# Performance work log

Hardware: AMD Instinct MI355X
Metric: run time of the kernel (lower is better)

The kernel has to match this reference:

```python
import jax, jax.numpy as jnp
import numpy as np

B, T, S_ENC, D, H, E, K = 4, 1024, 64, 1024, 16, 8, 2
DK = D // H
HID = 4 * D
NEG = -65504.0
EPS = 1e-5


def rmsnorm(x, w):
    return w * (x * jax.lax.rsqrt(jnp.mean(x * x, axis=-1, keepdims=True) + EPS))


def mha(xq, xk, xv, mask, wq, wk, wv, wo):
    # linear (no bias): y = x @ W.T
    q = jnp.einsum('bsd,ed->bse', xq, wq).reshape(xq.shape[0], -1, H, DK).transpose(0, 2, 1, 3)
    k = jnp.einsum('bsd,ed->bse', xk, wk).reshape(xk.shape[0], -1, H, DK).transpose(0, 2, 1, 3)
    v = jnp.einsum('bsd,ed->bse', xv, wv).reshape(xv.shape[0], -1, H, DK).transpose(0, 2, 1, 3)
    scores = jnp.einsum('bhqd,bhkd->bhqk', q, k) / jnp.sqrt(jnp.float32(DK))
    scores = jnp.where(mask[:, None, :, :] == 0, NEG, scores)
    attn = jax.nn.softmax(scores, axis=-1)
    out = jnp.einsum('bhqk,bhkd->bhqd', attn, v)
    out = out.transpose(0, 2, 1, 3).reshape(xq.shape[0], -1, D)
    return jnp.einsum('bsd,ed->bse', out, wo)


def moe_ffn(x, gate_w, exp_w1, exp_w2, sh_w1, sh_w2):
    b, s, d = x.shape
    xf = x.reshape(-1, d)                                     # [N, D]
    # shared expert
    sh = jnp.einsum('nd,hd->nh', xf, sh_w1)
    sh = jax.nn.silu(sh)
    sh = jnp.einsum('nh,dh->nd', sh, sh_w2)
    # gating
    logits = jnp.einsum('nd,ed->ne', xf, gate_w)              # [N, E]
    topk_vals, topk_idx = jax.lax.top_k(logits, K)
    topk_gates = jax.nn.softmax(topk_vals, axis=-1)
    n = xf.shape[0]
    gates = jnp.zeros((n, E), dtype=xf.dtype).at[jnp.arange(n)[:, None], topk_idx].set(topk_gates)
    # all experts computed densely (as in the torch code), then gated
    h = jnp.einsum('nd,ehd->neh', xf, exp_w1)                 # [N, E, 4D]
    h = jax.nn.silu(h)
    eo = jnp.einsum('neh,edh->ned', h, exp_w2)                # [N, E, D]
    sel = jnp.einsum('ned,ne->nd', eo, gates)
    return (sh + sel).reshape(b, s, d)


def setup_inputs() -> dict:
    key = jax.random.key(0)
    ks = jax.random.split(key, 16)
    sd = 1.0 / np.sqrt(D)
    inp = {
        'x': jax.random.normal(ks[0], (B, T, D), jnp.float32),
        'encoder_output': jax.random.normal(ks[1], (B, S_ENC, D), jnp.float32),
        'tgt_mask': jnp.tril(jnp.ones((T, T), jnp.int32))[None].repeat(B, 0),
        'src_mask': jnp.ones((B, T, S_ENC), jnp.int32),
        'norm1_w': jnp.ones((D,), jnp.float32),
        'norm2_w': jnp.ones((D,), jnp.float32),
        'norm3_w': jnp.ones((D,), jnp.float32),
        'sa_wq': jax.random.normal(ks[2], (D, D), jnp.float32) * sd,
        'sa_wk': jax.random.normal(ks[3], (D, D), jnp.float32) * sd,
        'sa_wv': jax.random.normal(ks[4], (D, D), jnp.float32) * sd,
        'sa_wo': jax.random.normal(ks[5], (D, D), jnp.float32) * sd,
        'ca_wq': jax.random.normal(ks[6], (D, D), jnp.float32) * sd,
        'ca_wk': jax.random.normal(ks[7], (D, D), jnp.float32) * sd,
        'ca_wv': jax.random.normal(ks[8], (D, D), jnp.float32) * sd,
        'ca_wo': jax.random.normal(ks[9], (D, D), jnp.float32) * sd,
        'gate_w': jax.random.normal(ks[10], (E, D), jnp.float32) * 0.02,
        'exp_w1': jax.random.normal(ks[11], (E, HID, D), jnp.float32) * sd,
        'exp_w2': jax.random.normal(ks[12], (E, D, HID), jnp.float32) / np.sqrt(HID),
        'sh_w1': jax.random.normal(ks[13], (HID, D), jnp.float32) * sd,
        'sh_w2': jax.random.normal(ks[14], (D, HID), jnp.float32) / np.sqrt(HID),
    }
    return inp


def reference(x, encoder_output, tgt_mask, src_mask, norm1_w, norm2_w, norm3_w,
              sa_wq, sa_wk, sa_wv, sa_wo, ca_wq, ca_wk, ca_wv, ca_wo,
              gate_w, exp_w1, exp_w2, sh_w1, sh_w2):
    xn = rmsnorm(x, norm1_w)
    h = x + mha(xn, xn, xn, tgt_mask, sa_wq, sa_wk, sa_wv, sa_wo)
    hn = rmsnorm(h, norm2_w)
    h = h + mha(hn, encoder_output, encoder_output, src_mask, ca_wq, ca_wk, ca_wv, ca_wo)
    hn = rmsnorm(h, norm3_w)
    return h + moe_ffn(hn, gate_w, exp_w1, exp_w2, sh_w1, sh_w2)
```

## Files before the change

### kernel.cpp

```cpp
#include <hip/hip_runtime.h>
#include <hip/hip_bf16.h>
#include <cstdint>
#include <cstddef>
#include <math.h>

typedef __attribute__((ext_vector_type(8))) short bf16x8;
typedef __attribute__((ext_vector_type(4))) float f32x4;
typedef __attribute__((ext_vector_type(4))) short s16x4;

static __device__ __forceinline__ short f2bf(float f) {
  union { __hip_bfloat16 b; short s; } u;
  u.b = __float2bfloat16(f);
  return u.s;
}

static __device__ __forceinline__ float bf2f(short s) {
  union { unsigned u; float f; } v;
  v.u = ((unsigned)(unsigned short)s) << 16;
  return v.f;
}

static __device__ __forceinline__ void gload_lds16(const short* g, short* l) {
  __builtin_amdgcn_global_load_lds((const __attribute__((address_space(1))) void*)g,
                                   (__attribute__((address_space(3))) void*)l,
                                   16, 0, 0);
}

__global__ __launch_bounds__(256) void cvt_k(const float* __restrict__ src,
                                             short* __restrict__ dst, long n4) {
  long i = (long)blockIdx.x * blockDim.x + threadIdx.x;
  long stride = (long)gridDim.x * blockDim.x;
  for (; i < n4; i += stride) {
    float4 v = ((const float4*)src)[i];
    s16x4 o;
    o.x = f2bf(v.x); o.y = f2bf(v.y); o.z = f2bf(v.z); o.w = f2bf(v.w);
    ((s16x4*)dst)[i] = o;
  }
}

__global__ __launch_bounds__(256) void cvt2_k(const float* __restrict__ src,
                                              short* __restrict__ hi,
                                              short* __restrict__ lo, long n4) {
  long i = (long)blockIdx.x * blockDim.x + threadIdx.x;
  long stride = (long)gridDim.x * blockDim.x;
  for (; i < n4; i += stride) {
    float4 v = ((const float4*)src)[i];
    s16x4 h, l;
    h.x = f2bf(v.x); l.x = f2bf(v.x - bf2f(h.x));
    h.y = f2bf(v.y); l.y = f2bf(v.y - bf2f(h.y));
    h.z = f2bf(v.z); l.z = f2bf(v.z - bf2f(h.z));
    h.w = f2bf(v.w); l.w = f2bf(v.w - bf2f(h.w));
    ((s16x4*)hi)[i] = h;
    ((s16x4*)lo)[i] = l;
  }
}

__global__ __launch_bounds__(256) void rms2_k(const float* __restrict__ x,
                                              const float* __restrict__ w,
                                              short* __restrict__ hi,
                                              short* __restrict__ lo) {
  const int row = blockIdx.x, tid = threadIdx.x;
  const float* xr = x + (size_t)row * 1024;
  float4 v = *(const float4*)&xr[tid * 4];
  float ss = v.x * v.x + v.y * v.y + v.z * v.z + v.w * v.w;
#pragma unroll
  for (int off = 32; off; off >>= 1) ss += __shfl_down(ss, off);
  __shared__ float red[4];
  if ((tid & 63) == 0) red[tid >> 6] = ss;
  __syncthreads();
  float rs = rsqrtf((red[0] + red[1] + red[2] + red[3]) * (1.f / 1024.f) + 1e-5f);
  float4 wv = *(const float4*)&w[tid * 4];
  float o0 = v.x * rs * wv.x, o1 = v.y * rs * wv.y;
  float o2 = v.z * rs * wv.z, o3 = v.w * rs * wv.w;
  s16x4 h, l;
  h.x = f2bf(o0); l.x = f2bf(o0 - bf2f(h.x));
  h.y = f2bf(o1); l.y = f2bf(o1 - bf2f(h.y));
  h.z = f2bf(o2); l.z = f2bf(o2 - bf2f(h.z));
  h.w = f2bf(o3); l.w = f2bf(o3 - bf2f(h.w));
  const size_t ib = (size_t)row * 1024 + tid * 4;
  *(s16x4*)&hi[ib] = h;
  *(s16x4*)&lo[ib] = l;
}

__global__ __launch_bounds__(256) void rms_k(const float* __restrict__ x,
                                             const float* __restrict__ w,
                                             short* __restrict__ obf) {
  const int row = blockIdx.x, tid = threadIdx.x;
  const float* xr = x + (size_t)row * 1024;
  float4 v = *(const float4*)&xr[tid * 4];
  float ss = v.x * v.x + v.y * v.y + v.z * v.z + v.w * v.w;
#pragma unroll
  for (int off = 32; off; off >>= 1) ss += __shfl_down(ss, off);
  __shared__ float red[4];
  if ((tid & 63) == 0) red[tid >> 6] = ss;
  __syncthreads();
  float rs = rsqrtf((red[0] + red[1] + red[2] + red[3]) * (1.f / 1024.f) + 1e-5f);
  float4 wv = *(const float4*)&w[tid * 4];
  s16x4 ob;
  ob.x = f2bf(v.x * rs * wv.x); ob.y = f2bf(v.y * rs * wv.y);
  ob.z = f2bf(v.z * rs * wv.z); ob.w = f2bf(v.w * rs * wv.w);
  *(s16x4*)&obf[(size_t)row * 1024 + tid * 4] = ob;
}

template <int EPI>
__global__ __launch_bounds__(256)
void gemm3_k(const short* __restrict__ Ah, const short* __restrict__ Al,
             const short* __restrict__ Bh, const short* __restrict__ Bl,
             float* __restrict__ C, const float* __restrict__ resid,
             short* __restrict__ Ch, short* __restrict__ Cl,
             int M, int N, int K) {
  __shared__ short sAh[128 * 32];
  __shared__ short sAl[128 * 32];
  __shared__ short sBh[128 * 32];
  __shared__ short sBl[128 * 32];

  const int bn = blockIdx.x, bm = blockIdx.y;
  const int tid = threadIdx.x;
  const int lane = tid & 63, wv = tid >> 6;
  const int rch = lane >> 2, cch = (lane & 3) << 3;
  const int wr = wv >> 1, wc = wv & 1;
  const int lr = lane & 15, lg = lane >> 4;
  const int c0 = wv * 2, c1 = wv * 2 + 1;

  const int ra0 = bm * 128 + c0 * 16 + rch;
  const int ra1 = bm * 128 + c1 * 16 + rch;
  const int rb0 = bn * 128 + c0 * 16 + rch, rb1 = bn * 128 + c1 * 16 + rch;

  f32x4 acc[4][4];
#pragma unroll
  for (int m = 0; m < 4; m++)
#pragma unroll
    for (int n = 0; n < 4; n++) acc[m][n] = (f32x4){0.f, 0.f, 0.f, 0.f};

  const int nk = K >> 5;
  for (int kt = 0; kt < nk; ++kt) {
    __syncthreads();
    const int colk = (kt << 5) + cch;
    gload_lds16(Ah + (size_t)ra0 * K + colk, &sAh[c0 * 512]);
    gload_lds16(Ah + (size_t)ra1 * K + colk, &sAh[c1 * 512]);
    gload_lds16(Al + (size_t)ra0 * K + colk, &sAl[c0 * 512]);
    gload_lds16(Al + (size_t)ra1 * K + colk, &sAl[c1 * 512]);
    gload_lds16(Bh + (size_t)rb0 * K + colk, &sBh[c0 * 512]);
    gload_lds16(Bh + (size_t)rb1 * K + colk, &sBh[c1 * 512]);
    gload_lds16(Bl + (size_t)rb0 * K + colk, &sBl[c0 * 512]);
    gload_lds16(Bl + (size_t)rb1 * K + colk, &sBl[c1 * 512]);
    __syncthreads();
    bf16x8 ah[4], al[4], bh[4], bl[4];
#pragma unroll
    for (int m = 0; m < 4; m++) {
      const int o = (wr * 64 + m * 16 + lr) * 32 + lg * 8;
      ah[m] = *(const bf16x8*)&sAh[o];
      al[m] = *(const bf16x8*)&sAl[o];
    }
#pragma unroll
    for (int n = 0; n < 4; n++) {
      const int o = (wc * 64 + n * 16 + lr) * 32 + lg * 8;
      bh[n] = *(const bf16x8*)&sBh[o];
      bl[n] = *(const bf16x8*)&sBl[o];
    }
#pragma unroll
    for (int m = 0; m < 4; m++)
#pragma unroll
      for (int n = 0; n < 4; n++) {
        acc[m][n] = __builtin_amdgcn_mfma_f32_16x16x32_bf16(ah[m], bh[n], acc[m][n], 0, 0, 0);
        acc[m][n] = __builtin_amdgcn_mfma_f32_16x16x32_bf16(al[m], bh[n], acc[m][n], 0, 0, 0);
        acc[m][n] = __builtin_amdgcn_mfma_f32_16x16x32_bf16(ah[m], bl[n], acc[m][n], 0, 0, 0);
      }
  }

  const int cbase = bn * 128 + wc * 64;
#pragma unroll
  for (int m = 0; m < 4; m++) {
    const int rl = bm * 128 + wr * 64 + m * 16 + lg * 4;
#pragma unroll
    for (int n = 0; n < 4; n++) {
      f32x4 v = acc[m][n];
      const int col = cbase + n * 16 + lr;
#pragma unroll
      for (int j = 0; j < 4; j++) {
        const size_t idx = (size_t)(rl + j) * N + col;
        if (EPI == 0) {
          C[idx] = v[j];
        } else if (EPI == 2) {
          C[idx] = v[j] + resid[idx];
        } else {
          short hh = f2bf(v[j]);
          Ch[idx] = hh;
          Cl[idx] = f2bf(v[j] - bf2f(hh));
        }
      }
    }
  }
}

template <bool CAUSAL>
__global__ __launch_bounds__(256)
void attn3_k(const short* __restrict__ Qh, const short* __restrict__ Ql, int ldq,
             const short* __restrict__ Kh, const short* __restrict__ Kl, int ldk,
             const short* __restrict__ Vh, const short* __restrict__ Vl, int ldv,
             short* __restrict__ Oh, short* __restrict__ Ol, int ldo,
             int Tq, int Tkv, float scale) {
  __shared__ short sQh[64 * 64], sQl[64 * 64];
  __shared__ short sKh[64 * 64], sKl[64 * 64];
  __shared__ short sVh[64 * 72], sVl[64 * 72];
  __shared__ short sPh[4][16 * 72], sPl[4][16 * 72];

  const int idx = blockIdx.x;
  const int qb = 15 - (idx >> 6);
  const int h = (idx >> 2) & 15;
  const int b = idx & 3;
  const int tid = threadIdx.x, lane = tid & 63, wv = tid >> 6;
  const int hoff = h * 64;
  const int lr = lane & 15, lg = lane >> 4;
  const int qlo = wv * 16;

#pragma unroll
  for (int j = 0; j < 2; j++) {
    int c = j * 256 + tid;
    int row = c >> 3, col = (c & 7) << 3;
    size_t g = (size_t)(b * Tq + qb * 64 + row) * ldq + hoff + col;
    *(bf16x8*)&sQh[row * 64 + col] = *(const bf16x8*)&Qh[g];
    *(bf16x8*)&sQl[row * 64 + col] = *(const bf16x8*)&Ql[g];
  }

  float m_run = -1e30f, l_run = 0.f;
  f32x4 o[4];
#pragma unroll
  for (int n = 0; n < 4; n++) o[n] = (f32x4){0.f, 0.f, 0.f, 0.f};

  const int ntiles = CAUSAL ? (qb + 1) : (Tkv >> 6);
  for (int kt = 0; kt < ntiles; ++kt) {
    __syncthreads();
#pragma unroll
    for (int j = 0; j < 2; j++) {
      int c = j * 256 + tid;
      int row = c >> 3, col = (c & 7) << 3;
      size_t gk = (size_t)(b * Tkv + kt * 64 + row) * ldk + hoff + col;
      *(bf16x8*)&sKh[row * 64 + col] = *(const bf16x8*)&Kh[gk];
      *(bf16x8*)&sKl[row * 64 + col] = *(const bf16x8*)&Kl[gk];
      size_t gv = (size_t)(b * Tkv + kt * 64 + row) * ldv + hoff + col;
      bf16x8 vh = *(const bf16x8*)&Vh[gv];
      bf16x8 vl = *(const bf16x8*)&Vl[gv];
#pragma unroll
      for (int i = 0; i < 8; i++) {
        sVh[(col + i) * 72 + row] = vh[i];
        sVl[(col + i) * 72 + row] = vl[i];
      }
    }
    __syncthreads();

    f32x4 st[4];
#pragma unroll
    for (int jk = 0; jk < 4; jk++) st[jk] = (f32x4){0.f, 0.f, 0.f, 0.f};
#pragma unroll
    for (int ks = 0; ks < 2; ks++) {
      bf16x8 qh = *(const bf16x8*)&sQh[(qlo + lr) * 64 + ks * 32 + lg * 8];
      bf16x8 ql = *(const bf16x8*)&sQl[(qlo + lr) * 64 + ks * 32 + lg * 8];
#pragma unroll
      for (int jk = 0; jk < 4; jk++) {
        const int o2 = (jk * 16 + lr) * 64 + ks * 32 + lg * 8;
        bf16x8 kh = *(const bf16x8*)&sKh[o2];
        bf16x8 kl = *(const bf16x8*)&sKl[o2];
        st[jk] = __builtin_amdgcn_mfma_f32_16x16x32_bf16(kh, qh, st[jk], 0, 0, 0);
        st[jk] = __builtin_amdgcn_mfma_f32_16x16x32_bf16(kl, qh, st[jk], 0, 0, 0);
        st[jk] = __builtin_amdgcn_mfma_f32_16x16x32_bf16(kh, ql, st[jk], 0, 0, 0);
      }
    }

    const int qg = qb * 64 + qlo + lr;
    float s[16];
    float tmax = -1e30f;
#pragma unroll
    for (int jk = 0; jk < 4; jk++)
#pragma unroll
      for (int r2 = 0; r2 < 4; r2++) {
        float xv = st[jk][r2] * scale;
        if (CAUSAL && kt == qb) {
          int kvidx = kt * 64 + jk * 16 + lg * 4 + r2;
          if (kvidx > qg) xv = -1e30f;
        }
        s[jk * 4 + r2] = xv;
        tmax = fmaxf(tmax, xv);
      }
    tmax = fmaxf(tmax, __shfl_xor(tmax, 16));
    tmax = fmaxf(tmax, __shfl_xor(tmax, 32));
    float m_new = fmaxf(m_run, tmax);
    float alpha = __expf(m_run - m_new);
    float tsum = 0.f;
#pragma unroll
    for (int i = 0; i < 16; i++) {
      float ev = (s[i] <= -1e29f) ? 0.f : __expf(s[i] - m_new);
      s[i] = ev;
      tsum += ev;
    }
    tsum += __shfl_xor(tsum, 16);
    tsum += __shfl_xor(tsum, 32);
    l_run = l_run * alpha + tsum;
    m_run = m_new;

    short* pwh = &sPh[wv][0];
    short* pwl = &sPl[wv][0];
#pragma unroll
    for (int jk = 0; jk < 4; jk++) {
      s16x4 ph, pl;
      float e0 = s[jk * 4 + 0], e1 = s[jk * 4 + 1], e2 = s[jk * 4 + 2], e3 = s[jk * 4 + 3];
      ph.x = f2bf(e0); pl.x = f2bf(e0 - bf2f(ph.x));
      ph.y = f2bf(e1); pl.y = f2bf(e1 - bf2f(ph.y));
      ph.z = f2bf(e2); pl.z = f2bf(e2 - bf2f(ph.z));
      ph.w = f2bf(e3); pl.w = f2bf(e3 - bf2f(ph.w));
      *(s16x4*)&pwh[lr * 72 + jk * 16 + lg * 4] = ph;
      *(s16x4*)&pwl[lr * 72 + jk * 16 + lg * 4] = pl;
    }
#pragma unroll
    for (int r2 = 0; r2 < 4; r2++) {
      float al = __shfl(alpha, lg * 4 + r2);
#pragma unroll
      for (int db = 0; db < 4; db++) o[db][r2] *= al;
    }
    __syncthreads();

#pragma unroll
    for (int ks = 0; ks < 2; ks++) {
      bf16x8 pah = *(const bf16x8*)&pwh[lr * 72 + ks * 32 + lg * 8];
      bf16x8 pal = *(const bf16x8*)&pwl[lr * 72 + ks * 32 + lg * 8];
#pragma unroll
      for (int db = 0; db < 4; db++) {
        const int o2 = (db * 16 + lr) * 72 + ks * 32 + lg * 8;
        bf16x8 vfh = *(const bf16x8*)&sVh[o2];
        bf16x8 vfl = *(const bf16x8*)&sVl[o2];
        o[db] = __builtin_amdgcn_mfma_f32_16x16x32_bf16(pah, vfh, o[db], 0, 0, 0);
        o[db] = __builtin_amdgcn_mfma_f32_16x16x32_bf16(pal, vfh, o[db], 0, 0, 0);
        o[db] = __builtin_amdgcn_mfma_f32_16x16x32_bf16(pah, vfl, o[db], 0, 0, 0);
      }
    }
  }

  float rinv = 1.f / l_run;
#pragma unroll
  for (int r2 = 0; r2 < 4; r2++) {
    float inv = __shfl(rinv, lg * 4 + r2);
    int token = b * Tq + qb * 64 + qlo + lg * 4 + r2;
#pragma unroll
    for (int db = 0; db < 4; db++) {
      float vv = o[db][r2] * inv;
      short hh = f2bf(vv);
      const size_t ob = (size_t)token * ldo + hoff + db * 16 + lr;
      Oh[ob] = hh;
      Ol[ob] = f2bf(vv - bf2f(hh));
    }
  }
}

template <int EPI, int MODE>
__global__ __launch_bounds__(256)
void gemm_bt_k(const short* __restrict__ A, const short* __restrict__ B,
               void* C, int M, int N, int K,
               const int* __restrict__ row_map,
               const int* __restrict__ counts,
               const int* __restrict__ offs, int e0) {
  __shared__ short sA[128 * 32];
  __shared__ short sB[128 * 32];
  __shared__ int sRow[128];

  const int tid = threadIdx.x;
  const int bn = blockIdx.x, bm = blockIdx.y;
  const int e = e0 + blockIdx.z;
  const int cnt = counts[e];
  const int base = offs[e];
  if (bm * 128 >= cnt) return;
  const short* Bp = B + (size_t)e * N * K;

  const int lane = tid & 63, wv = tid >> 6;
  const int rch = lane >> 2, cch = (lane & 3) << 3;
  const int wr = wv >> 1, wc = wv & 1;
  const int lr = lane & 15, lg = lane >> 4;
  const int c0 = wv * 2, c1 = wv * 2 + 1;

  int ra0, ra1;
  if (MODE == 2) {
    int rl0 = bm * 128 + c0 * 16 + rch, rl1 = bm * 128 + c1 * 16 + rch;
    ra0 = base + ((rl0 < cnt) ? rl0 : 0);
    ra1 = base + ((rl1 < cnt) ? rl1 : 0);
  } else {
    if (tid < 128) {
      int r = bm * 128 + tid;
      sRow[tid] = (r < cnt) ? row_map[base + r] : row_map[base];
    }
    __syncthreads();
    ra0 = sRow[c0 * 16 + rch];
    ra1 = sRow[c1 * 16 + rch];
  }
  const int rb0 = bn * 128 + c0 * 16 + rch, rb1 = bn * 128 + c1 * 16 + rch;

  f32x4 acc[4][4];
#pragma unroll
  for (int m = 0; m < 4; m++)
#pragma unroll
    for (int n = 0; n < 4; n++) acc[m][n] = (f32x4){0.f, 0.f, 0.f, 0.f};

  const int nk = K >> 5;
  for (int kt = 0; kt < nk; ++kt) {
    __syncthreads();
    const int colk = (kt << 5) + cch;
    gload_lds16(A + (size_t)ra0 * K + colk, &sA[c0 * 512]);
    gload_lds16(A + (size_t)ra1 * K + colk, &sA[c1 * 512]);
    gload_lds16(Bp + (size_t)rb0 * K + colk, &sB[c0 * 512]);
    gload_lds16(Bp + (size_t)rb1 * K + colk, &sB[c1 * 512]);
    __syncthreads();
    bf16x8 a[4], b[4];
#pragma unroll
    for (int m = 0; m < 4; m++) a[m] = *(const bf16x8*)&sA[(wr * 64 + m * 16 + lr) * 32 + lg * 8];
#pragma unroll
    for (int n = 0; n < 4; n++) b[n] = *(const bf16x8*)&sB[(wc * 64 + n * 16 + lr) * 32 + lg * 8];
#pragma unroll
    for (int m = 0; m < 4; m++)
#pragma unroll
      for (int n = 0; n < 4; n++)
        acc[m][n] = __builtin_amdgcn_mfma_f32_16x16x32_bf16(a[m], b[n], acc[m][n], 0, 0, 0);
  }

  const int cbase = bn * 128 + wc * 64;
#pragma unroll
  for (int m = 0; m < 4; m++) {
    const int rl = wr * 64 + m * 16 + lg * 4;
#pragma unroll
    for (int n = 0; n < 4; n++) {
      f32x4 v = acc[m][n];
      const int col = cbase + n * 16 + lr;
#pragma unroll
      for (int j = 0; j < 4; j++) {
        const int rloc = bm * 128 + rl + j;
        if (rloc >= cnt) continue;
        const size_t idx = (size_t)(base + rloc) * N + col;
        float xv = v[j];
        if (EPI == 1) {
          float s = xv / (1.f + __expf(-xv));
          ((short*)C)[idx] = f2bf(s);
        } else {
          ((short*)C)[idx] = f2bf(xv);
        }
      }
    }
  }
}

__global__ __launch_bounds__(256) void gate_k(const float* __restrict__ H,
                                              const float* __restrict__ w3,
                                              const float* __restrict__ gw,
                                              int* counts, int* tok_e, int* tok_s,
                                              float* tok_g) {
  const int token = blockIdx.x * 4 + (threadIdx.x >> 6);
  const int lane = threadIdx.x & 63;
  const float* xr = H + (size_t)token * 1024;
  double a[8] = {0, 0, 0, 0, 0, 0, 0, 0};
  double ss = 0.0;
#pragma unroll
  for (int i = 0; i < 4; i++) {
    float4 xv = *(const float4*)&xr[i * 256 + lane * 4];
    float4 w3v = *(const float4*)&w3[i * 256 + lane * 4];
    ss += (double)xv.x * xv.x + (double)xv.y * xv.y + (double)xv.z * xv.z + (double)xv.w * xv.w;
    double xw0 = (double)xv.x * (double)w3v.x, xw1 = (double)xv.y * (double)w3v.y;
    double xw2 = (double)xv.z * (double)w3v.z, xw3 = (double)xv.w * (double)w3v.w;
#pragma unroll
    for (int e = 0; e < 8; e++) {
      float4 wv = *(const float4*)&gw[e * 1024 + i * 256 + lane * 4];
      a[e] += xw0 * wv.x + xw1 * wv.y + xw2 * wv.z + xw3 * wv.w;
    }
  }
#pragma unroll
  for (int off = 32; off; off >>= 1) {
    ss += __shfl_down(ss, off);
#pragma unroll
    for (int e = 0; e < 8; e++) a[e] += __shfl_down(a[e], off);
  }
  if (lane == 0) {
    double v0 = a[0]; int i0 = 0;
#pragma unroll
    for (int e = 1; e < 8; e++) if (a[e] > v0) { v0 = a[e]; i0 = e; }
    double v1 = -1e300; int i1 = 0;
#pragma unroll
    for (int e = 0; e < 8; e++) if (e != i0 && a[e] > v1) { v1 = a[e]; i1 = e; }
    double rs = 1.0 / sqrt(ss * (1.0 / 1024.0) + 1e-5);
    double t = exp((v1 - v0) * rs);
    double g0 = 1.0 / (1.0 + t);
    int s0 = atomicAdd(&counts[i0], 1);
    int s1 = atomicAdd(&counts[i1], 1);
    tok_e[2 * token] = i0; tok_e[2 * token + 1] = i1;
    tok_s[2 * token] = s0; tok_s[2 * token + 1] = s1;
    tok_g[2 * token] = (float)g0; tok_g[2 * token + 1] = (float)(1.0 - g0);
  }
}

__global__ void offsets_k(int* counts, int* offs) {
  if (threadIdx.x == 0 && blockIdx.x == 0) {
    counts[8] = 4096;
    int s = 0;
    for (int e = 0; e < 9; e++) { offs[e] = s; s += counts[e]; }
  }
}

__global__ __launch_bounds__(256) void build_rows_k(const int* __restrict__ offs,
                                                    const int* __restrict__ tok_e,
                                                    const int* __restrict__ tok_s,
                                                    int* __restrict__ row_map,
                                                    int* __restrict__ tok_row) {
  int n = blockIdx.x * 256 + threadIdx.x;
  int e0 = tok_e[2 * n], e1 = tok_e[2 * n + 1];
  int r0 = offs[e0] + tok_s[2 * n], r1 = offs[e1] + tok_s[2 * n + 1];
  row_map[r0] = n; row_map[r1] = n;
  row_map[8192 + n] = n;
  tok_row[2 * n] = r0; tok_row[2 * n + 1] = r1;
}

__global__ __launch_bounds__(256) void combine_k(const float* __restrict__ H,
                                                 const short* __restrict__ eo,
                                                 const int* __restrict__ tok_row,
                                                 const float* __restrict__ tok_g,
                                                 float* __restrict__ out) {
  const int n = blockIdx.x, t = threadIdx.x;
  const int r0 = tok_row[2 * n], r1 = tok_row[2 * n + 1];
  const float g0 = tok_g[2 * n], g1 = tok_g[2 * n + 1];
  const size_t ib = (size_t)n * 1024 + t * 4;
  float4 hv = *(const float4*)&H[ib];
  s16x4 sv = *(const s16x4*)&eo[(size_t)(8192 + n) * 1024 + t * 4];
  s16x4 a0 = *(const s16x4*)&eo[(size_t)r0 * 1024 + t * 4];
  s16x4 a1 = *(const s16x4*)&eo[(size_t)r1 * 1024 + t * 4];
  float4 ov;
  ov.x = hv.x + bf2f(sv.x) + g0 * bf2f(a0.x) + g1 * bf2f(a1.x);
  ov.y = hv.y + bf2f(sv.y) + g0 * bf2f(a0.y) + g1 * bf2f(a1.y);
  ov.z = hv.z + bf2f(sv.z) + g0 * bf2f(a0.z) + g1 * bf2f(a1.z);
  ov.w = hv.w + bf2f(sv.w) + g0 * bf2f(a0.w) + g1 * bf2f(a1.w);
  *(float4*)&out[ib] = ov;
}

extern "C" void kernel_launch(void* const* d_in, const int* in_sizes, int n_in,
                              void* d_out, int out_size, void* d_ws, size_t ws_size,
                              hipStream_t stream) {
  (void)in_sizes; (void)n_in; (void)out_size;
  const float* x     = (const float*)d_in[0];
  const float* enc   = (const float*)d_in[1];
  const float* n1w   = (const float*)d_in[4];
  const float* n2w   = (const float*)d_in[5];
  const float* n3w   = (const float*)d_in[6];
  const float* sa_wq = (const float*)d_in[7];
  const float* sa_wk = (const float*)d_in[8];
  const float* sa_wv = (const float*)d_in[9];
  const float* sa_wo = (const float*)d_in[10];
  const float* ca_wq = (const float*)d_in[11];
  const float* ca_wk = (const float*)d_in[12];
  const float* ca_wv = (const float*)d_in[13];
  const float* ca_wo = (const float*)d_in[14];
  const float* gw    = (const float*)d_in[15];
  const float* e_w1  = (const float*)d_in[16];
  const float* e_w2  = (const float*)d_in[17];
  const float* s_w1  = (const float*)d_in[18];
  const float* s_w2  = (const float*)d_in[19];
  float* out = (float*)d_out;

  char* p = (char*)d_ws;
  size_t off = 0;
  auto alloc = [&](size_t bytes) -> void* {
    void* r = p + off;
    off += (bytes + 255) & ~(size_t)255;
    return r;
  };
  short* w_all1 = (short*)alloc(9LL * 4096 * 1024 * 2);
  short* w_all2 = (short*)alloc(9LL * 1024 * 4096 * 2);
  short* xn     = (short*)alloc(4096LL * 1024 * 2);
  char*  U      = (char*)alloc(12288LL * 4096 * 2);
  short* hbuf   = (short*)U;
  float* Hb     = (float*)alloc(4096LL * 1024 * 4);
  short* eo     = (short*)alloc(12288LL * 1024 * 2);
  short* xh     = (short*)alloc(4096LL * 1024 * 2);
  short* xl     = (short*)alloc(4096LL * 1024 * 2);
  short* ench   = (short*)alloc(256LL * 1024 * 2);
  short* encl   = (short*)alloc(256LL * 1024 * 2);
  short* wsh    = (short*)alloc(3072LL * 1024 * 2);
  short* wsl    = (short*)alloc(3072LL * 1024 * 2);
  int*   counts = (int*)alloc(9 * 4);
  int*   offs   = (int*)alloc(9 * 4);
  int*   tok_e  = (int*)alloc(4096LL * 2 * 4);
  int*   tok_s  = (int*)alloc(4096LL * 2 * 4);
  float* tok_g  = (float*)alloc(4096LL * 2 * 4);
  int*   tok_row= (int*)alloc(4096LL * 2 * 4);
  int*   row_map= (int*)alloc(12288LL * 4);
  if (off > ws_size) return;

  short* qkvh = (short*)U;
  short* qkvl = qkvh + 4096LL * 3072;
  short* crossQh = (short*)U;
  short* crossQl = crossQh + 4096LL * 1024;
  short* encKVh  = crossQl + 4096LL * 1024;
  short* encKVl  = encKVh + 256LL * 2048;

  auto cvt = [&](const float* s, short* d, long n) {
    long n4 = n / 4;
    long g = (n4 + 255) / 256;
    int grid = (int)(g > 4096 ? 4096 : g);
    cvt_k<<<grid, 256, 0, stream>>>(s, d, n4);
  };
  auto cvt2 = [&](const float* s, short* h, short* l, long n) {
    long n4 = n / 4;
    long g = (n4 + 255) / 256;
    int grid = (int)(g > 4096 ? 4096 : g);
    cvt2_k<<<grid, 256, 0, stream>>>(s, h, l, n4);
  };

  cvt(e_w1, w_all1, 8L * 4096 * 1024);
  cvt(s_w1, w_all1 + 8L * 4096 * 1024, 4096L * 1024);
  cvt(e_w2, w_all2, 8L * 1024 * 4096);
  cvt(s_w2, w_all2 + 8L * 1024 * 4096, 1024L * 4096);
  cvt2(enc, ench, encl, 256L * 1024);

  rms2_k<<<4096, 256, 0, stream>>>(x, n1w, xh, xl);
  cvt2(sa_wq, wsh, wsl, 1024L * 1024);
  cvt2(sa_wk, wsh + 1048576, wsl + 1048576, 1024L * 1024);
  cvt2(sa_wv, wsh + 2097152, wsl + 2097152, 1024L * 1024);
  gemm3_k<3><<<dim3(24, 32), 256, 0, stream>>>(xh, xl, wsh, wsl, nullptr, nullptr,
      qkvh, qkvl, 4096, 3072, 1024);
  attn3_k<true><<<1024, 256, 0, stream>>>(qkvh, qkvl, 3072,
      qkvh + 1024, qkvl + 1024, 3072, qkvh + 2048, qkvl + 2048, 3072,
      xh, xl, 1024, 1024, 1024, 0.125f);
  cvt2(sa_wo, wsh, wsl, 1024L * 1024);
  gemm3_k<2><<<dim3(8, 32), 256, 0, stream>>>(xh, xl, wsh, wsl, Hb, x,
      nullptr, nullptr, 4096, 1024, 1024);

  rms2_k<<<4096, 256, 0, stream>>>(Hb, n2w, xh, xl);
  cvt2(ca_wq, wsh, wsl, 1024L * 1024);
  gemm3_k<3><<<dim3(8, 32), 256, 0, stream>>>(xh, xl, wsh, wsl, nullptr, nullptr,
      crossQh, crossQl, 4096, 1024, 1024);
  cvt2(ca_wk, wsh, wsl, 1024L * 1024);
  cvt2(ca_wv, wsh + 1048576, wsl + 1048576, 1024L * 1024);
  gemm3_k<3><<<dim3(16, 2), 256, 0, stream>>>(ench, encl, wsh, wsl, nullptr, nullptr,
      encKVh, encKVl, 256, 2048, 1024);
  attn3_k<false><<<1024, 256, 0, stream>>>(crossQh, crossQl, 1024,
      encKVh, encKVl, 2048, encKVh + 1024, encKVl + 1024, 2048,
      xh, xl, 1024, 1024, 64, 0.125f);
  cvt2(ca_wo, wsh, wsl, 1024L * 1024);
  gemm3_k<2><<<dim3(8, 32), 256, 0, stream>>>(xh, xl, wsh, wsl, Hb, Hb,
      nullptr, nullptr, 4096, 1024, 1024);

  rms_k<<<4096, 256, 0, stream>>>(Hb, n3w, xn);
  hipMemsetAsync(counts, 0, 8 * sizeof(int), stream);
  gate_k<<<1024, 256, 0, stream>>>(Hb, n3w, gw, counts, tok_e, tok_s, tok_g);
  offsets_k<<<1, 1, 0, stream>>>(counts, offs);
  build_rows_k<<<16, 256, 0, stream>>>(offs, tok_e, tok_s, row_map, tok_row);
  gemm_bt_k<1, 1><<<dim3(32, 32, 4), 256, 0, stream>>>(xn, w_all1, hbuf,
      4096, 4096, 1024, row_map, counts, offs, 0);
  gemm_bt_k<3, 2><<<dim3(8, 32, 4), 256, 0, stream>>>(hbuf, w_all2, eo,
      4096, 1024, 4096, nullptr, counts, offs, 0);
  gemm_bt_k<1, 1><<<dim3(32, 32, 5), 256, 0, stream>>>(xn, w_all1, hbuf,
      4096, 4096, 1024, row_map, counts, offs, 4);
  gemm_bt_k<3, 2><<<dim3(8, 32, 5), 256, 0, stream>>>(hbuf, w_all2, eo,
      4096, 1024, 4096, nullptr, counts, offs, 4);

  combine_k<<<4096, 256, 0, stream>>>(Hb, eo, tok_row, tok_g, out);
}
```

Measured before the change: 1.115 ms.

## Pad expert segments to tile multiples and launch flat grouped MoE GEMMs

Expert row segments are padded to multiples of 128 so each M-tile belongs to exactly one expert. Each tile finds its expert by scanning the padded offsets, which lets the four per-expert-group GEMM launches become two flat launches. The per-row bounds checks in the loaders and epilogue go away. The cost is extra padding rows of wasted compute and an added memset of row_map so padding rows point at a valid token.

```diff
diff --git a/kernel.cpp b/kernel.cpp
--- a/kernel.cpp
+++ b/kernel.cpp
@@ -354,20 +354,19 @@
 template <int EPI, int MODE>
 __global__ __launch_bounds__(256)
 void gemm_bt_k(const short* __restrict__ A, const short* __restrict__ B,
-               void* C, int M, int N, int K,
+               void* C, int N, int K,
                const int* __restrict__ row_map,
-               const int* __restrict__ counts,
-               const int* __restrict__ offs, int e0) {
+               const int* __restrict__ offsP) {
   __shared__ short sA[128 * 32];
   __shared__ short sB[128 * 32];
   __shared__ int sRow[128];
 
   const int tid = threadIdx.x;
   const int bn = blockIdx.x, bm = blockIdx.y;
-  const int e = e0 + blockIdx.z;
-  const int cnt = counts[e];
-  const int base = offs[e];
-  if (bm * 128 >= cnt) return;
+  const int row0 = bm * 128;
+  if (row0 >= offsP[9]) return;
+  int e = 0;
+  while (row0 >= offsP[e + 1]) ++e;
   const short* Bp = B + (size_t)e * N * K;
 
   const int lane = tid & 63, wv = tid >> 6;
@@ -378,14 +377,10 @@
 
   int ra0, ra1;
   if (MODE == 2) {
-    int rl0 = bm * 128 + c0 * 16 + rch, rl1 = bm * 128 + c1 * 16 + rch;
-    ra0 = base + ((rl0 < cnt) ? rl0 : 0);
-    ra1 = base + ((rl1 < cnt) ? rl1 : 0);
+    ra0 = row0 + c0 * 16 + rch;
+    ra1 = row0 + c1 * 16 + rch;
   } else {
-    if (tid < 128) {
-      int r = bm * 128 + tid;
-      sRow[tid] = (r < cnt) ? row_map[base + r] : row_map[base];
-    }
+    if (tid < 128) sRow[tid] = row_map[row0 + tid];
     __syncthreads();
     ra0 = sRow[c0 * 16 + rch];
     ra1 = sRow[c1 * 16 + rch];
@@ -422,16 +417,14 @@
   const int cbase = bn * 128 + wc * 64;
 #pragma unroll
   for (int m = 0; m < 4; m++) {
-    const int rl = wr * 64 + m * 16 + lg * 4;
+    const int rl = row0 + wr * 64 + m * 16 + lg * 4;
 #pragma unroll
     for (int n = 0; n < 4; n++) {
       f32x4 v = acc[m][n];
       const int col = cbase + n * 16 + lr;
 #pragma unroll
       for (int j = 0; j < 4; j++) {
-        const int rloc = bm * 128 + rl + j;
-        if (rloc >= cnt) continue;
-        const size_t idx = (size_t)(base + rloc) * N + col;
+        const size_t idx = (size_t)(rl + j) * N + col;
         float xv = v[j];
         if (EPI == 1) {
           float s = xv / (1.f + __expf(-xv));
@@ -491,24 +484,28 @@
   }
 }
 
-__global__ void offsets_k(int* counts, int* offs) {
+__global__ void offsets_k(const int* counts, int* offsP) {
   if (threadIdx.x == 0 && blockIdx.x == 0) {
-    counts[8] = 4096;
     int s = 0;
-    for (int e = 0; e < 9; e++) { offs[e] = s; s += counts[e]; }
-  }
-}
-
-__global__ __launch_bounds__(256) void build_rows_k(const int* __restrict__ offs,
+    for (int e = 0; e < 8; e++) {
+      offsP[e] = s;
+      s += (counts[e] + 127) & ~127;
+    }
+    offsP[8] = s;
+    offsP[9] = s + 4096;
+  }
+}
+
+__global__ __launch_bounds__(256) void build_rows_k(const int* __restrict__ offsP,
                                                     const int* __restrict__ tok_e,
                                                     const int* __restrict__ tok_s,
                                                     int* __restrict__ row_map,
                                                     int* __restrict__ tok_row) {
   int n = blockIdx.x * 256 + threadIdx.x;
   int e0 = tok_e[2 * n], e1 = tok_e[2 * n + 1];
-  int r0 = offs[e0] + tok_s[2 * n], r1 = offs[e1] + tok_s[2 * n + 1];
+  int r0 = offsP[e0] + tok_s[2 * n], r1 = offsP[e1] + tok_s[2 * n + 1];
   row_map[r0] = n; row_map[r1] = n;
-  row_map[8192 + n] = n;
+  row_map[offsP[8] + n] = n;
   tok_row[2 * n] = r0; tok_row[2 * n + 1] = r1;
 }
 
@@ -516,13 +513,15 @@
                                                  const short* __restrict__ eo,
                                                  const int* __restrict__ tok_row,
                                                  const float* __restrict__ tok_g,
+                                                 const int* __restrict__ offsP,
                                                  float* __restrict__ out) {
   const int n = blockIdx.x, t = threadIdx.x;
   const int r0 = tok_row[2 * n], r1 = tok_row[2 * n + 1];
+  const int rs = offsP[8] + n;
   const float g0 = tok_g[2 * n], g1 = tok_g[2 * n + 1];
   const size_t ib = (size_t)n * 1024 + t * 4;
   float4 hv = *(const float4*)&H[ib];
-  s16x4 sv = *(const s16x4*)&eo[(size_t)(8192 + n) * 1024 + t * 4];
+  s16x4 sv = *(const s16x4*)&eo[(size_t)rs * 1024 + t * 4];
   s16x4 a0 = *(const s16x4*)&eo[(size_t)r0 * 1024 + t * 4];
   s16x4 a1 = *(const s16x4*)&eo[(size_t)r1 * 1024 + t * 4];
   float4 ov;
@@ -557,6 +556,8 @@
   const float* s_w2  = (const float*)d_in[19];
   float* out = (float*)d_out;
 
+  const int MAXROWS = 13440;
+
   char* p = (char*)d_ws;
   size_t off = 0;
   auto alloc = [&](size_t bytes) -> void* {
@@ -567,23 +568,23 @@
   short* w_all1 = (short*)alloc(9LL * 4096 * 1024 * 2);
   short* w_all2 = (short*)alloc(9LL * 1024 * 4096 * 2);
   short* xn     = (short*)alloc(4096LL * 1024 * 2);
-  char*  U      = (char*)alloc(12288LL * 4096 * 2);
+  char*  U      = (char*)alloc((size_t)MAXROWS * 4096 * 2);
   short* hbuf   = (short*)U;
   float* Hb     = (float*)alloc(4096LL * 1024 * 4);
-  short* eo     = (short*)alloc(12288LL * 1024 * 2);
+  short* eo     = (short*)alloc((size_t)MAXROWS * 1024 * 2);
   short* xh     = (short*)alloc(4096LL * 1024 * 2);
   short* xl     = (short*)alloc(4096LL * 1024 * 2);
   short* ench   = (short*)alloc(256LL * 1024 * 2);
   short* encl   = (short*)alloc(256LL * 1024 * 2);
   short* wsh    = (short*)alloc(3072LL * 1024 * 2);
   short* wsl    = (short*)alloc(3072LL * 1024 * 2);
-  int*   counts = (int*)alloc(9 * 4);
-  int*   offs   = (int*)alloc(9 * 4);
+  int*   counts = (int*)alloc(8 * 4);
+  int*   offsP  = (int*)alloc(10 * 4);
   int*   tok_e  = (int*)alloc(4096LL * 2 * 4);
   int*   tok_s  = (int*)alloc(4096LL * 2 * 4);
   float* tok_g  = (float*)alloc(4096LL * 2 * 4);
   int*   tok_row= (int*)alloc(4096LL * 2 * 4);
-  int*   row_map= (int*)alloc(12288LL * 4);
+  int*   row_map= (int*)alloc((size_t)MAXROWS * 4);
   if (off > ws_size) return;
 
   short* qkvh = (short*)U;
@@ -642,17 +643,14 @@
 
   rms_k<<<4096, 256, 0, stream>>>(Hb, n3w, xn);
   hipMemsetAsync(counts, 0, 8 * sizeof(int), stream);
+  hipMemsetAsync(row_map, 0, (size_t)MAXROWS * 4, stream);
   gate_k<<<1024, 256, 0, stream>>>(Hb, n3w, gw, counts, tok_e, tok_s, tok_g);
-  offsets_k<<<1, 1, 0, stream>>>(counts, offs);
-  build_rows_k<<<16, 256, 0, stream>>>(offs, tok_e, tok_s, row_map, tok_row);
-  gemm_bt_k<1, 1><<<dim3(32, 32, 4), 256, 0, stream>>>(xn, w_all1, hbuf,
-      4096, 4096, 1024, row_map, counts, offs, 0);
-  gemm_bt_k<3, 2><<<dim3(8, 32, 4), 256, 0, stream>>>(hbuf, w_all2, eo,
-      4096, 1024, 4096, nullptr, counts, offs, 0);
-  gemm_bt_k<1, 1><<<dim3(32, 32, 5), 256, 0, stream>>>(xn, w_all1, hbuf,
-      4096, 4096, 1024, row_map, counts, offs, 4);
-  gemm_bt_k<3, 2><<<dim3(8, 32, 5), 256, 0, stream>>>(hbuf, w_all2, eo,
-      4096, 1024, 4096, nullptr, counts, offs, 4);
-
-  combine_k<<<4096, 256, 0, stream>>>(Hb, eo, tok_row, tok_g, out);
-}
+  offsets_k<<<1, 1, 0, stream>>>(counts, offsP);
+  build_rows_k<<<16, 256, 0, stream>>>(offsP, tok_e, tok_s, row_map, tok_row);
+  gemm_bt_k<1, 1><<<dim3(32, MAXROWS / 128), 256, 0, stream>>>(xn, w_all1, hbuf,
+      4096, 1024, row_map, offsP);
+  gemm_bt_k<3, 2><<<dim3(8, MAXROWS / 128), 256, 0, stream>>>(hbuf, w_all2, eo,
+      1024, 4096, nullptr, offsP);
+
+  combine_k<<<4096, 256, 0, stream>>>(Hb, eo, tok_row, tok_g, offsP, out);
+}
```

New measurement: 1.057 ms. -5.2%, faster.

## Widen MoE GEMM K-tile to 64 with XOR-swizzled LDS and merge expert launches

Applied to the files above, without the earlier changes.

The grouped expert GEMM now stages a 128x64 K-slice per iteration instead of 128x32. Each wave loads rows as 8 lanes per row, with the column chunk XOR-swizzled by row to avoid LDS bank conflicts on the MFMA fragment reads. This halves the number of barrier pairs per K loop and adds two MFMA sub-steps per tile. The two launches per GEMM (experts 0-3 and 4-8) are merged into a single 9-expert grid, which removes launch overhead and the tail between launches. The cost is twice the LDS per block, which may lower occupancy.

```diff
diff --git a/kernel.cpp b/kernel.cpp
--- a/kernel.cpp
+++ b/kernel.cpp
@@ -357,40 +357,43 @@
                void* C, int M, int N, int K,
                const int* __restrict__ row_map,
                const int* __restrict__ counts,
-               const int* __restrict__ offs, int e0) {
-  __shared__ short sA[128 * 32];
-  __shared__ short sB[128 * 32];
+               const int* __restrict__ offs) {
+  __shared__ short sA[128 * 64];
+  __shared__ short sB[128 * 64];
   __shared__ int sRow[128];
 
   const int tid = threadIdx.x;
   const int bn = blockIdx.x, bm = blockIdx.y;
-  const int e = e0 + blockIdx.z;
+  const int e = blockIdx.z;
   const int cnt = counts[e];
   const int base = offs[e];
   if (bm * 128 >= cnt) return;
   const short* Bp = B + (size_t)e * N * K;
 
   const int lane = tid & 63, wv = tid >> 6;
-  const int rch = lane >> 2, cch = (lane & 3) << 3;
+  const int lrow = lane >> 3;
+  const int lcc = ((lane & 7) ^ lrow) << 3;
   const int wr = wv >> 1, wc = wv & 1;
   const int lr = lane & 15, lg = lane >> 4;
-  const int c0 = wv * 2, c1 = wv * 2 + 1;
-
-  int ra0, ra1;
-  if (MODE == 2) {
-    int rl0 = bm * 128 + c0 * 16 + rch, rl1 = bm * 128 + c1 * 16 + rch;
-    ra0 = base + ((rl0 < cnt) ? rl0 : 0);
-    ra1 = base + ((rl1 < cnt) ? rl1 : 0);
-  } else {
+
+  if (MODE == 1) {
     if (tid < 128) {
       int r = bm * 128 + tid;
       sRow[tid] = (r < cnt) ? row_map[base + r] : row_map[base];
     }
     __syncthreads();
-    ra0 = sRow[c0 * 16 + rch];
-    ra1 = sRow[c1 * 16 + rch];
-  }
-  const int rb0 = bn * 128 + c0 * 16 + rch, rb1 = bn * 128 + c1 * 16 + rch;
+  }
+  int rag[4], rbg[4];
+#pragma unroll
+  for (int i = 0; i < 4; i++) {
+    const int rl = wv * 32 + i * 8 + lrow;
+    if (MODE == 2) {
+      rag[i] = base + ((bm * 128 + rl < cnt) ? (bm * 128 + rl) : 0);
+    } else {
+      rag[i] = sRow[rl];
+    }
+    rbg[i] = bn * 128 + rl;
+  }
 
   f32x4 acc[4][4];
 #pragma unroll
@@ -398,25 +401,35 @@
 #pragma unroll
     for (int n = 0; n < 4; n++) acc[m][n] = (f32x4){0.f, 0.f, 0.f, 0.f};
 
-  const int nk = K >> 5;
+  const int nk = K >> 6;
   for (int kt = 0; kt < nk; ++kt) {
     __syncthreads();
-    const int colk = (kt << 5) + cch;
-    gload_lds16(A + (size_t)ra0 * K + colk, &sA[c0 * 512]);
-    gload_lds16(A + (size_t)ra1 * K + colk, &sA[c1 * 512]);
-    gload_lds16(Bp + (size_t)rb0 * K + colk, &sB[c0 * 512]);
-    gload_lds16(Bp + (size_t)rb1 * K + colk, &sB[c1 * 512]);
-    __syncthreads();
-    bf16x8 a[4], b[4];
-#pragma unroll
-    for (int m = 0; m < 4; m++) a[m] = *(const bf16x8*)&sA[(wr * 64 + m * 16 + lr) * 32 + lg * 8];
-#pragma unroll
-    for (int n = 0; n < 4; n++) b[n] = *(const bf16x8*)&sB[(wc * 64 + n * 16 + lr) * 32 + lg * 8];
-#pragma unroll
-    for (int m = 0; m < 4; m++)
-#pragma unroll
-      for (int n = 0; n < 4; n++)
-        acc[m][n] = __builtin_amdgcn_mfma_f32_16x16x32_bf16(a[m], b[n], acc[m][n], 0, 0, 0);
+    const int colk = (kt << 6) + lcc;
+#pragma unroll
+    for (int i = 0; i < 4; i++) {
+      gload_lds16(A + (size_t)rag[i] * K + colk, &sA[(wv * 32 + i * 8) * 64]);
+      gload_lds16(Bp + (size_t)rbg[i] * K + colk, &sB[(wv * 32 + i * 8) * 64]);
+    }
+    __syncthreads();
+#pragma unroll
+    for (int ks = 0; ks < 2; ks++) {
+      bf16x8 a[4], b[4];
+#pragma unroll
+      for (int m = 0; m < 4; m++) {
+        const int rr = wr * 64 + m * 16 + lr;
+        a[m] = *(const bf16x8*)&sA[rr * 64 + ((((ks << 2) + lg) ^ (lr & 7)) << 3)];
+      }
+#pragma unroll
+      for (int n = 0; n < 4; n++) {
+        const int rr = wc * 64 + n * 16 + lr;
+        b[n] = *(const bf16x8*)&sB[rr * 64 + ((((ks << 2) + lg) ^ (lr & 7)) << 3)];
+      }
+#pragma unroll
+      for (int m = 0; m < 4; m++)
+#pragma unroll
+        for (int n = 0; n < 4; n++)
+          acc[m][n] = __builtin_amdgcn_mfma_f32_16x16x32_bf16(a[m], b[n], acc[m][n], 0, 0, 0);
+    }
   }
 
   const int cbase = bn * 128 + wc * 64;
@@ -645,14 +658,10 @@
   gate_k<<<1024, 256, 0, stream>>>(Hb, n3w, gw, counts, tok_e, tok_s, tok_g);
   offsets_k<<<1, 1, 0, stream>>>(counts, offs);
   build_rows_k<<<16, 256, 0, stream>>>(offs, tok_e, tok_s, row_map, tok_row);
-  gemm_bt_k<1, 1><<<dim3(32, 32, 4), 256, 0, stream>>>(xn, w_all1, hbuf,
-      4096, 4096, 1024, row_map, counts, offs, 0);
-  gemm_bt_k<3, 2><<<dim3(8, 32, 4), 256, 0, stream>>>(hbuf, w_all2, eo,
-      4096, 1024, 4096, nullptr, counts, offs, 0);
-  gemm_bt_k<1, 1><<<dim3(32, 32, 5), 256, 0, stream>>>(xn, w_all1, hbuf,
-      4096, 4096, 1024, row_map, counts, offs, 4);
-  gemm_bt_k<3, 2><<<dim3(8, 32, 5), 256, 0, stream>>>(hbuf, w_all2, eo,
-      4096, 1024, 4096, nullptr, counts, offs, 4);
+  gemm_bt_k<1, 1><<<dim3(32, 32, 9), 256, 0, stream>>>(xn, w_all1, hbuf,
+      4096, 4096, 1024, row_map, counts, offs);
+  gemm_bt_k<3, 2><<<dim3(8, 32, 9), 256, 0, stream>>>(hbuf, w_all2, eo,
+      4096, 1024, 4096, row_map, counts, offs);
 
   combine_k<<<4096, 256, 0, stream>>>(Hb, eo, tok_row, tok_g, out);
 }
```

Result: faster. 990.2 us (-11.2%).
